# Performance work log

Hardware: AMD Instinct MI355X
Metric: run time of the kernel (lower is better)

Reference implementation:

```python
import jax, jax.numpy as jnp
import numpy as np

B, S, D, H = 4, 2048, 1024, 16
HD = D // H

def setup_inputs() -> dict:
    key = jax.random.key(0)
    ks = jax.random.split(key, 9)
    s = 1.0 / np.sqrt(D)
    return {
        "x": jax.random.normal(ks[0], (B, S, D), dtype=jnp.float32),
        "wq": jax.random.normal(ks[1], (D, D), dtype=jnp.float32) * s,
        "bq": jnp.zeros((D,), dtype=jnp.float32),
        "wk": jax.random.normal(ks[2], (D, D), dtype=jnp.float32) * s,
        "bk": jnp.zeros((D,), dtype=jnp.float32),
        "wv": jax.random.normal(ks[3], (D, D), dtype=jnp.float32) * s,
        "bv": jnp.zeros((D,), dtype=jnp.float32),
        "wo": jax.random.normal(ks[4], (D, D), dtype=jnp.float32) * s,
        "bo": jnp.zeros((D,), dtype=jnp.float32),
    }

def reference(x, wq, bq, wk, bk, wv, bv, wo, bo):
    # QKV projections, split heads: [B,S,D] -> [B,H,S,HD]
    def split_heads(t):
        return t.reshape(B, S, H, HD).transpose(0, 2, 1, 3)
    q = split_heads(x @ wq + bq)
    k = split_heads(x @ wk + bk)
    v = split_heads(x @ wv + bv)
    # scaled dot-product attention with full score matrix [B,H,S,S]
    scores = jnp.einsum("bhqd,bhkd->bhqk", q, k) / jnp.sqrt(jnp.float32(HD))
    weights = jax.nn.softmax(scores, axis=-1)
    attn = jnp.einsum("bhqk,bhkd->bhqd", weights, v)
    # merge heads and output projection
    out = attn.transpose(0, 2, 1, 3).reshape(B, S, D) @ wo + bo
    return out
```

## Files before the change

kernel.cpp:

```cpp
#include <hip/hip_runtime.h>
#include <hip/hip_bf16.h>


#define B_  4
#define S_  2048
#define D_  1024
#define H_  16
#define HD_ 64
#define M_  (B_*S_)
#define QSCALE (0.125f * 1.4426950408889634f)

typedef __attribute__((ext_vector_type(8))) short short8;
typedef __attribute__((ext_vector_type(4))) float f32x4;
typedef __hip_bfloat16 bf16;

__device__ inline void gload_lds16(const void* g, void* l) {
  __builtin_amdgcn_global_load_lds(
      (const __attribute__((address_space(1))) void*)g,
      (__attribute__((address_space(3))) void*)l,
      16, 0, 0);
}

__device__ inline f32x4 mfma16(short8 a, short8 b, f32x4 c) {
  return __builtin_amdgcn_mfma_f32_16x16x32_bf16(a, b, c, 0, 0, 0);
}

__device__ inline short bfbits(float f) {
  bf16 h = (bf16)f;
  return *reinterpret_cast<short*>(&h);
}

__global__ void convert_x_kernel(const float* __restrict__ x, bf16* __restrict__ xb) {
  const int i = (blockIdx.x * 256 + threadIdx.x) * 8;
  float4 a = *reinterpret_cast<const float4*>(x + i);
  float4 b = *reinterpret_cast<const float4*>(x + i + 4);
  bf16 o[8];
  o[0] = (bf16)a.x; o[1] = (bf16)a.y; o[2] = (bf16)a.z; o[3] = (bf16)a.w;
  o[4] = (bf16)b.x; o[5] = (bf16)b.y; o[6] = (bf16)b.z; o[7] = (bf16)b.w;
  *reinterpret_cast<int4*>(xb + i) = *reinterpret_cast<const int4*>(o);
}

struct TP { const float* w[4]; bf16* wt[4]; };

__global__ void transpose_w_kernel(TP p) {
  const float* w = p.w[blockIdx.z];
  bf16* wt = p.wt[blockIdx.z];
  __shared__ float t[32][33];
  const int k0 = blockIdx.y * 32, n0 = blockIdx.x * 32;
  const int c = threadIdx.x & 31, r4 = threadIdx.x >> 5;
  #pragma unroll
  for (int i = 0; i < 4; ++i) {
    int r = r4 + i * 8;
    t[r][c] = w[(size_t)(k0 + r) * D_ + n0 + c];
  }
  __syncthreads();
  #pragma unroll
  for (int i = 0; i < 4; ++i) {
    int r = r4 + i * 8;
    wt[(size_t)(n0 + r) * D_ + k0 + c] = (bf16)t[c][r];
  }
}

__global__ __launch_bounds__(256) void gemm_qkv_kernel(
    const bf16* __restrict__ A, const bf16* __restrict__ Bt3,
    const float* __restrict__ bq, const float* __restrict__ bk,
    const float* __restrict__ bv,
    bf16* __restrict__ qb, bf16* __restrict__ kb, bf16* __restrict__ vtb)
{
  constexpr int BK = 32;
  __shared__ __align__(16) bf16 As[128 * BK];
  __shared__ __align__(16) bf16 Bs[128 * BK];
  const int tid = threadIdx.x;
  const int w = tid >> 6, l = tid & 63;
  const int lo = l & 15, hi = l >> 4;
  const int wm = w >> 1, wn = w & 1;
  const int row0 = blockIdx.y * 128;
  const int col0 = blockIdx.x * 128;

  f32x4 acc[4][4] = {};

  for (int kt = 0; kt < D_; kt += BK) {
    __syncthreads();
    #pragma unroll
    for (int i = 0; i < 2; ++i) {
      const int cb = i * 256 + w * 64;
      const int c  = cb + l;
      gload_lds16(A   + (size_t)(row0 + (c >> 2)) * D_ + kt + (c & 3) * 8,
                  (void*)(As + cb * 8));
      gload_lds16(Bt3 + (size_t)(col0 + (c >> 2)) * D_ + kt + (c & 3) * 8,
                  (void*)(Bs + cb * 8));
    }
    __syncthreads();

    short8 a[4], b[4];
    #pragma unroll
    for (int m = 0; m < 4; ++m)
      a[m] = *reinterpret_cast<const short8*>(As + (wm*64 + m*16 + lo) * BK + hi*8);
    #pragma unroll
    for (int n = 0; n < 4; ++n)
      b[n] = *reinterpret_cast<const short8*>(Bs + (wn*64 + n*16 + lo) * BK + hi*8);
    #pragma unroll
    for (int m = 0; m < 4; ++m)
      #pragma unroll
      for (int n = 0; n < 4; ++n)
        acc[m][n] = mfma16(a[m], b[n], acc[m][n]);
  }

  #pragma unroll
  for (int n = 0; n < 4; ++n) {
    const int c3 = col0 + wn*64 + n*16 + lo;
    const int which = c3 >> 10;
    const int cc = c3 & 1023;
    const int h = cc >> 6, hd = cc & 63;
    const float* bias = (which == 0) ? bq : (which == 1) ? bk : bv;
    const float bvv = bias[cc];
    #pragma unroll
    for (int m = 0; m < 4; ++m) {
      #pragma unroll
      for (int j = 0; j < 4; ++j) {
        const int r = row0 + wm*64 + m*16 + hi*4 + j;
        const int bb = r >> 11, s = r & (S_ - 1);
        float v = acc[m][n][j] + bvv;
        if (which == 0) {
          v *= QSCALE;
          qb[((size_t)(bb * H_ + h) * S_ + s) * HD_ + hd] = (bf16)v;
        } else if (which == 1) {
          kb[((size_t)(bb * H_ + h) * S_ + s) * HD_ + hd] = (bf16)v;
        } else {
          vtb[((size_t)(bb * H_ + h) * HD_ + hd) * S_ + s] = (bf16)v;
        }
      }
    }
  }
}

__global__ __launch_bounds__(256) void gemm_out_kernel(
    const bf16* __restrict__ A, const bf16* __restrict__ Bt,
    const float* __restrict__ bias, float* __restrict__ out)
{
  constexpr int BK = 32;
  __shared__ __align__(16) bf16 As[64 * BK];
  __shared__ __align__(16) bf16 Bs[128 * BK];
  const int tid = threadIdx.x;
  const int w = tid >> 6, l = tid & 63;
  const int lo = l & 15, hi = l >> 4;
  const int wm = w >> 1, wn = w & 1;
  const int row0 = blockIdx.y * 64;
  const int col0 = blockIdx.x * 128;

  f32x4 acc[2][4] = {};

  for (int kt = 0; kt < D_; kt += BK) {
    __syncthreads();
    #pragma unroll
    for (int i = 0; i < 2; ++i) {
      const int cb = i * 256 + w * 64;
      const int c  = cb + l;
      if (i == 0)
        gload_lds16(A + (size_t)(row0 + (c >> 2)) * D_ + kt + (c & 3) * 8,
                    (void*)(As + cb * 8));
      gload_lds16(Bt + (size_t)(col0 + (c >> 2)) * D_ + kt + (c & 3) * 8,
                  (void*)(Bs + cb * 8));
    }
    __syncthreads();

    short8 a[2], b[4];
    #pragma unroll
    for (int m = 0; m < 2; ++m)
      a[m] = *reinterpret_cast<const short8*>(As + (wm*32 + m*16 + lo) * BK + hi*8);
    #pragma unroll
    for (int n = 0; n < 4; ++n)
      b[n] = *reinterpret_cast<const short8*>(Bs + (wn*64 + n*16 + lo) * BK + hi*8);
    #pragma unroll
    for (int m = 0; m < 2; ++m)
      #pragma unroll
      for (int n = 0; n < 4; ++n)
        acc[m][n] = mfma16(a[m], b[n], acc[m][n]);
  }

  #pragma unroll
  for (int n = 0; n < 4; ++n) {
    const int c = col0 + wn*64 + n*16 + lo;
    const float bvv = bias[c];
    #pragma unroll
    for (int m = 0; m < 2; ++m) {
      #pragma unroll
      for (int j = 0; j < 4; ++j) {
        const int r = row0 + wm*32 + m*16 + hi*4 + j;
        out[(size_t)r * D_ + c] = acc[m][n][j] + bvv;
      }
    }
  }
}

__global__ __launch_bounds__(256, 4) void attn_kernel(
    const bf16* __restrict__ q, const bf16* __restrict__ k,
    const bf16* __restrict__ vt, bf16* __restrict__ ao)
{
  __shared__ __align__(16) bf16 Kl[64 * 72];
  __shared__ __align__(16) bf16 Vtl[64 * 72];

  const int tid = threadIdx.x;
  const int w = tid >> 6, l = tid & 63;
  const int lo = l & 15, hi = l >> 4;
  const int flat = blockIdx.x;
  const int L = (flat & 7) * 128 + (flat >> 3);
  const int bh = L >> 4;
  const int q0 = (L & 15) * 128 + w * 32;

  const bf16* kbase = k  + (size_t)bh * S_ * HD_;
  const bf16* vbase = vt + (size_t)bh * HD_ * S_;

  short8 bq[2][2];
  const size_t qrow = (size_t)bh * S_ + q0;
  #pragma unroll
  for (int n = 0; n < 2; ++n)
    #pragma unroll
    for (int kk = 0; kk < 2; ++kk)
      bq[n][kk] = *reinterpret_cast<const short8*>(
          q + (qrow + n*16 + lo) * HD_ + kk*32 + hi*8);

  f32x4 o[4][2] = {};
  float mrun[2], lrun[2];
  #pragma unroll
  for (int n = 0; n < 2; ++n) { mrun[n] = -1.0e30f; lrun[n] = 0.0f; }

  const int r0 = tid >> 3,         co0 = (tid & 7) * 8;
  const int r1 = (tid + 256) >> 3, co1 = (tid & 7) * 8;

  int4 kreg0, kreg1, vreg0, vreg1;
  kreg0 = *reinterpret_cast<const int4*>(kbase + (size_t)r0 * HD_ + co0);
  kreg1 = *reinterpret_cast<const int4*>(kbase + (size_t)r1 * HD_ + co1);
  vreg0 = *reinterpret_cast<const int4*>(vbase + (size_t)r0 * S_ + co0);
  vreg1 = *reinterpret_cast<const int4*>(vbase + (size_t)r1 * S_ + co1);

  for (int kt = 0; kt < S_; kt += 64) {
    __syncthreads();
    *reinterpret_cast<int4*>(Kl  + r0*72 + co0) = kreg0;
    *reinterpret_cast<int4*>(Kl  + r1*72 + co1) = kreg1;
    *reinterpret_cast<int4*>(Vtl + r0*72 + co0) = vreg0;
    *reinterpret_cast<int4*>(Vtl + r1*72 + co1) = vreg1;
    if (kt + 64 < S_) {
      const int nt = kt + 64;
      kreg0 = *reinterpret_cast<const int4*>(kbase + (size_t)(nt + r0) * HD_ + co0);
      kreg1 = *reinterpret_cast<const int4*>(kbase + (size_t)(nt + r1) * HD_ + co1);
      vreg0 = *reinterpret_cast<const int4*>(vbase + (size_t)r0 * S_ + nt + co0);
      vreg1 = *reinterpret_cast<const int4*>(vbase + (size_t)r1 * S_ + nt + co1);
    }
    __syncthreads();

    f32x4 s[4][2] = {};
    __builtin_amdgcn_s_setprio(1);
    #pragma unroll
    for (int m = 0; m < 4; ++m) {
      short8 kf0 = *reinterpret_cast<const short8*>(Kl + (m*16+lo)*72 + hi*8);
      short8 kf1 = *reinterpret_cast<const short8*>(Kl + (m*16+lo)*72 + 32 + hi*8);
      #pragma unroll
      for (int n = 0; n < 2; ++n) {
        s[m][n] = mfma16(kf0, bq[n][0], s[m][n]);
        s[m][n] = mfma16(kf1, bq[n][1], s[m][n]);
      }
    }
    __builtin_amdgcn_s_setprio(0);

    short8 pb[2][2];
    #pragma unroll
    for (int n = 0; n < 2; ++n) {
      float t0 = fmaxf(fmaxf(s[0][n][0], s[0][n][1]), s[0][n][2]);
      float t1 = fmaxf(fmaxf(s[0][n][3], s[1][n][0]), s[1][n][1]);
      float t2 = fmaxf(fmaxf(s[1][n][2], s[1][n][3]), s[2][n][0]);
      float t3 = fmaxf(fmaxf(s[2][n][1], s[2][n][2]), s[2][n][3]);
      float t4 = fmaxf(fmaxf(s[3][n][0], s[3][n][1]), s[3][n][2]);
      float mx = fmaxf(fmaxf(fmaxf(t0, t1), fmaxf(t2, t3)),
                       fmaxf(t4, s[3][n][3]));
      mx = fmaxf(mx, __shfl_xor(mx, 16, 64));
      mx = fmaxf(mx, __shfl_xor(mx, 32, 64));
      float mn;
      if (__all(mx <= mrun[n] + 8.0f)) {
        mn = mrun[n];
      } else {
        mn = fmaxf(mrun[n], mx);
        const float corr = exp2f(mrun[n] - mn);
        lrun[n] *= corr;
        #pragma unroll
        for (int mm = 0; mm < 4; ++mm)
          #pragma unroll
          for (int j = 0; j < 4; ++j)
            o[mm][n][j] *= corr;
        mrun[n] = mn;
      }
      float sum = 0.0f;
      #pragma unroll
      for (int m = 0; m < 4; ++m)
        #pragma unroll
        for (int j = 0; j < 4; ++j) {
          const float p = exp2f(s[m][n][j] - mn);
          s[m][n][j] = p;
          sum += p;
        }
      sum += __shfl_xor(sum, 16, 64);
      sum += __shfl_xor(sum, 32, 64);
      lrun[n] += sum;
      #pragma unroll
      for (int kk = 0; kk < 2; ++kk) {
        short8 t;
        t[0] = bfbits(s[2*kk][n][0]);   t[1] = bfbits(s[2*kk][n][1]);
        t[2] = bfbits(s[2*kk][n][2]);   t[3] = bfbits(s[2*kk][n][3]);
        t[4] = bfbits(s[2*kk+1][n][0]); t[5] = bfbits(s[2*kk+1][n][1]);
        t[6] = bfbits(s[2*kk+1][n][2]); t[7] = bfbits(s[2*kk+1][n][3]);
        pb[n][kk] = t;
      }
    }

    __builtin_amdgcn_s_setprio(1);
    #pragma unroll
    for (int mm = 0; mm < 4; ++mm) {
      short8 vf[2];
      #pragma unroll
      for (int kk = 0; kk < 2; ++kk) {
        union { short8 v; uint2 u2[2]; } x;
        x.u2[0] = *reinterpret_cast<const uint2*>(Vtl + (mm*16+lo)*72 + kk*32 + hi*4);
        x.u2[1] = *reinterpret_cast<const uint2*>(Vtl + (mm*16+lo)*72 + kk*32 + 16 + hi*4);
        vf[kk] = x.v;
      }
      #pragma unroll
      for (int n = 0; n < 2; ++n) {
        o[mm][n] = mfma16(vf[0], pb[n][0], o[mm][n]);
        o[mm][n] = mfma16(vf[1], pb[n][1], o[mm][n]);
      }
    }
    __builtin_amdgcn_s_setprio(0);
  }

  const int b = bh >> 4, h = bh & 15;
  #pragma unroll
  for (int n = 0; n < 2; ++n) {
    const float inv = 1.0f / lrun[n];
    const size_t row = (size_t)b * S_ + q0 + n*16 + lo;
    #pragma unroll
    for (int mm = 0; mm < 4; ++mm) {
      bf16 ov[4];
      #pragma unroll
      for (int j = 0; j < 4; ++j) ov[j] = (bf16)(o[mm][n][j] * inv);
      *reinterpret_cast<uint2*>(ao + row * D_ + h*64 + mm*16 + hi*4) =
          *reinterpret_cast<const uint2*>(ov);
    }
  }
}

extern "C" void kernel_launch(void* const* d_in, const int* in_sizes, int n_in,
                              void* d_out, int out_size, void* d_ws, size_t ws_size,
                              hipStream_t stream) {
  const float* x  = (const float*)d_in[0];
  const float* wq = (const float*)d_in[1];
  const float* bq = (const float*)d_in[2];
  const float* wk = (const float*)d_in[3];
  const float* bk = (const float*)d_in[4];
  const float* wv = (const float*)d_in[5];
  const float* bv = (const float*)d_in[6];
  const float* wo = (const float*)d_in[7];
  const float* bo = (const float*)d_in[8];

  char* ws = (char*)d_ws;
  bf16* xb  = (bf16*)(ws);
  bf16* wqt = (bf16*)(ws + ((size_t)16 << 20));
  bf16* wkt = (bf16*)(ws + ((size_t)18 << 20));
  bf16* wvt = (bf16*)(ws + ((size_t)20 << 20));
  bf16* wot = (bf16*)(ws + ((size_t)22 << 20));
  bf16* qb  = (bf16*)(ws + ((size_t)24 << 20));
  bf16* kb  = (bf16*)(ws + ((size_t)40 << 20));
  bf16* vtb = (bf16*)(ws + ((size_t)56 << 20));
  bf16* aob = (bf16*)(ws + ((size_t)72 << 20));

  convert_x_kernel<<<dim3((M_ * D_) / (256 * 8)), 256, 0, stream>>>(x, xb);

  TP p;
  p.w[0] = wq; p.w[1] = wk; p.w[2] = wv; p.w[3] = wo;
  p.wt[0] = wqt; p.wt[1] = wkt; p.wt[2] = wvt; p.wt[3] = wot;
  transpose_w_kernel<<<dim3(32, 32, 4), 256, 0, stream>>>(p);

  gemm_qkv_kernel<<<dim3(24, 64), 256, 0, stream>>>(
      xb, wqt, bq, bk, bv, qb, kb, vtb);

  attn_kernel<<<dim3(1024), 256, 0, stream>>>(qb, kb, vtb, aob);

  gemm_out_kernel<<<dim3(8, 128), 256, 0, stream>>>(aob, wot, bo, (float*)d_out);
}
```

Measured before the change: 340.5 us.

## Double-buffer attention K/V tiles via direct-to-LDS loads, larger query tile per wave

The attention kernel now loads K and V^T tiles straight into LDS with global_load_lds into two alternating buffers, using an XOR swizzle in place of the old padding. This drops the register staging and one barrier per iteration. Each wave now handles 64 query rows instead of 32, so every K/V tile is reused across twice as many queries, and the grid is halved to 512 blocks. The cost is more accumulator registers per thread (launch bounds no longer pin 4 blocks per CU), lower occupancy, and fewer blocks to spread across the CUs.

Result: slower. 418.0 us (+22.7%).

```diff
diff --git a/kernel.cpp b/kernel.cpp
--- a/kernel.cpp
+++ b/kernel.cpp
@@ -193,79 +193,85 @@
   }
 }
 
-__global__ __launch_bounds__(256, 4) void attn_kernel(
+__global__ __launch_bounds__(256) void attn_kernel(
     const bf16* __restrict__ q, const bf16* __restrict__ k,
     const bf16* __restrict__ vt, bf16* __restrict__ ao)
 {
-  __shared__ __align__(16) bf16 Kl[64 * 72];
-  __shared__ __align__(16) bf16 Vtl[64 * 72];
+  __shared__ __align__(16) bf16 Kl[2][64 * 64];
+  __shared__ __align__(16) bf16 Vtl[2][64 * 64];
 
   const int tid = threadIdx.x;
   const int w = tid >> 6, l = tid & 63;
   const int lo = l & 15, hi = l >> 4;
   const int flat = blockIdx.x;
-  const int L = (flat & 7) * 128 + (flat >> 3);
-  const int bh = L >> 4;
-  const int q0 = (L & 15) * 128 + w * 32;
+  const int L = (flat & 7) * 64 + (flat >> 3);
+  const int bh = L >> 3;
+  const int q0 = (L & 7) * 256 + w * 64;
 
   const bf16* kbase = k  + (size_t)bh * S_ * HD_;
   const bf16* vbase = vt + (size_t)bh * HD_ * S_;
 
-  short8 bq[2][2];
+  short8 bq[4][2];
   const size_t qrow = (size_t)bh * S_ + q0;
   #pragma unroll
-  for (int n = 0; n < 2; ++n)
+  for (int n = 0; n < 4; ++n)
     #pragma unroll
     for (int kk = 0; kk < 2; ++kk)
       bq[n][kk] = *reinterpret_cast<const short8*>(
           q + (qrow + n*16 + lo) * HD_ + kk*32 + hi*8);
 
-  f32x4 o[4][2] = {};
-  float mrun[2], lrun[2];
-  #pragma unroll
-  for (int n = 0; n < 2; ++n) { mrun[n] = -1.0e30f; lrun[n] = 0.0f; }
-
-  const int r0 = tid >> 3,         co0 = (tid & 7) * 8;
-  const int r1 = (tid + 256) >> 3, co1 = (tid & 7) * 8;
-
-  int4 kreg0, kreg1, vreg0, vreg1;
-  kreg0 = *reinterpret_cast<const int4*>(kbase + (size_t)r0 * HD_ + co0);
-  kreg1 = *reinterpret_cast<const int4*>(kbase + (size_t)r1 * HD_ + co1);
-  vreg0 = *reinterpret_cast<const int4*>(vbase + (size_t)r0 * S_ + co0);
-  vreg1 = *reinterpret_cast<const int4*>(vbase + (size_t)r1 * S_ + co1);
-
+  f32x4 o[4][4] = {};
+  float mrun[4], lrun[4];
+  #pragma unroll
+  for (int n = 0; n < 4; ++n) { mrun[n] = -1.0e30f; lrun[n] = 0.0f; }
+
+  const int sr = l >> 3;
+  const int ss = (l & 7) ^ sr;
+
+  const int r7 = lo & 7;
+
+  #pragma unroll
+  for (int i = 0; i < 2; ++i) {
+    const int cb = i * 2048 + w * 512;
+    const int r  = i * 32 + w * 8 + sr;
+    gload_lds16(kbase + (size_t)r * HD_ + ss*8, (void*)(&Kl[0][cb]));
+    gload_lds16(vbase + (size_t)r * S_  + ss*8, (void*)(&Vtl[0][cb]));
+  }
+  __syncthreads();
+
+  int cur = 0;
   for (int kt = 0; kt < S_; kt += 64) {
-    __syncthreads();
-    *reinterpret_cast<int4*>(Kl  + r0*72 + co0) = kreg0;
-    *reinterpret_cast<int4*>(Kl  + r1*72 + co1) = kreg1;
-    *reinterpret_cast<int4*>(Vtl + r0*72 + co0) = vreg0;
-    *reinterpret_cast<int4*>(Vtl + r1*72 + co1) = vreg1;
     if (kt + 64 < S_) {
       const int nt = kt + 64;
-      kreg0 = *reinterpret_cast<const int4*>(kbase + (size_t)(nt + r0) * HD_ + co0);
-      kreg1 = *reinterpret_cast<const int4*>(kbase + (size_t)(nt + r1) * HD_ + co1);
-      vreg0 = *reinterpret_cast<const int4*>(vbase + (size_t)r0 * S_ + nt + co0);
-      vreg1 = *reinterpret_cast<const int4*>(vbase + (size_t)r1 * S_ + nt + co1);
-    }
-    __syncthreads();
-
-    f32x4 s[4][2] = {};
+      #pragma unroll
+      for (int i = 0; i < 2; ++i) {
+        const int cb = i * 2048 + w * 512;
+        const int r  = i * 32 + w * 8 + sr;
+        gload_lds16(kbase + (size_t)(nt + r) * HD_ + ss*8, (void*)(&Kl[cur^1][cb]));
+        gload_lds16(vbase + (size_t)r * S_ + nt + ss*8,    (void*)(&Vtl[cur^1][cb]));
+      }
+    }
+    const bf16* Kb = &Kl[cur][0];
+    const bf16* Vb = &Vtl[cur][0];
+
+    f32x4 s[4][4] = {};
     __builtin_amdgcn_s_setprio(1);
     #pragma unroll
     for (int m = 0; m < 4; ++m) {
-      short8 kf0 = *reinterpret_cast<const short8*>(Kl + (m*16+lo)*72 + hi*8);
-      short8 kf1 = *reinterpret_cast<const short8*>(Kl + (m*16+lo)*72 + 32 + hi*8);
-      #pragma unroll
-      for (int n = 0; n < 2; ++n) {
+      const int row = m*16 + lo;
+      short8 kf0 = *reinterpret_cast<const short8*>(Kb + row*64 + ((hi     ^ r7) << 3));
+      short8 kf1 = *reinterpret_cast<const short8*>(Kb + row*64 + (((hi+4) ^ r7) << 3));
+      #pragma unroll
+      for (int n = 0; n < 4; ++n) {
         s[m][n] = mfma16(kf0, bq[n][0], s[m][n]);
         s[m][n] = mfma16(kf1, bq[n][1], s[m][n]);
       }
     }
     __builtin_amdgcn_s_setprio(0);
 
-    short8 pb[2][2];
-    #pragma unroll
-    for (int n = 0; n < 2; ++n) {
+    short8 pb[4][2];
+    #pragma unroll
+    for (int n = 0; n < 4; ++n) {
       float t0 = fmaxf(fmaxf(s[0][n][0], s[0][n][1]), s[0][n][2]);
       float t1 = fmaxf(fmaxf(s[0][n][3], s[1][n][0]), s[1][n][1]);
       float t2 = fmaxf(fmaxf(s[1][n][2], s[1][n][3]), s[2][n][0]);
@@ -315,26 +321,33 @@
     __builtin_amdgcn_s_setprio(1);
     #pragma unroll
     for (int mm = 0; mm < 4; ++mm) {
+      const int row = mm*16 + lo;
       short8 vf[2];
       #pragma unroll
       for (int kk = 0; kk < 2; ++kk) {
+        const int s1 = 4*kk + (hi >> 1);
+        const int p1 = s1 ^ r7, p2 = (s1 + 2) ^ r7;
+        const int sub = (hi & 1) * 4;
         union { short8 v; uint2 u2[2]; } x;
-        x.u2[0] = *reinterpret_cast<const uint2*>(Vtl + (mm*16+lo)*72 + kk*32 + hi*4);
-        x.u2[1] = *reinterpret_cast<const uint2*>(Vtl + (mm*16+lo)*72 + kk*32 + 16 + hi*4);
+        x.u2[0] = *reinterpret_cast<const uint2*>(Vb + row*64 + p1*8 + sub);
+        x.u2[1] = *reinterpret_cast<const uint2*>(Vb + row*64 + p2*8 + sub);
         vf[kk] = x.v;
       }
       #pragma unroll
-      for (int n = 0; n < 2; ++n) {
+      for (int n = 0; n < 4; ++n) {
         o[mm][n] = mfma16(vf[0], pb[n][0], o[mm][n]);
         o[mm][n] = mfma16(vf[1], pb[n][1], o[mm][n]);
       }
     }
     __builtin_amdgcn_s_setprio(0);
+
+    __syncthreads();
+    cur ^= 1;
   }
 
   const int b = bh >> 4, h = bh & 15;
   #pragma unroll
-  for (int n = 0; n < 2; ++n) {
+  for (int n = 0; n < 4; ++n) {
     const float inv = 1.0f / lrun[n];
     const size_t row = (size_t)b * S_ + q0 + n*16 + lo;
     #pragma unroll
@@ -382,7 +395,7 @@
   gemm_qkv_kernel<<<dim3(24, 64), 256, 0, stream>>>(
       xb, wqt, bq, bk, bv, qb, kb, vtb);
 
-  attn_kernel<<<dim3(1024), 256, 0, stream>>>(qb, kb, vtb, aob);
+  attn_kernel<<<dim3(512), 256, 0, stream>>>(qb, kb, vtb, aob);
 
   gemm_out_kernel<<<dim3(8, 128), 256, 0, stream>>>(aob, wot, bo, (float*)d_out);
 }
```
